# Optimization experiments

Hardware: AMD Instinct MI355X
Metric: run time of the kernel (lower is better)

Reference implementation:

```python
import jax, jax.numpy as jnp
import numpy as np
from jax import lax

DIM = 1152
HEADS = 16
HEAD_DIM = 72  # HEADS*HEAD_DIM == DIM
HID = 4608     # int(DIM*4.0)
B = 2
N = 4096
EPS_RMS = 1e-6
EPS_LA = 1e-15


def setup_inputs() -> dict:
    key = jax.random.key(0)
    ks = jax.random.split(key, 12)
    w = lambda k, shape: (jax.random.normal(k, shape, jnp.float32) * 0.02)
    z = lambda n: jnp.zeros((n,), jnp.float32)
    return {
        "hidden_states": jax.random.normal(ks[0], (B, N, DIM), jnp.float32),
        "temb": jax.random.normal(ks[1], (B, 6 * DIM), jnp.float32),
        "scale_shift_table": jax.random.normal(ks[2], (6, DIM), jnp.float32) / np.float32(np.sqrt(DIM)),
        "Wq": w(ks[3], (DIM, DIM)), "bq": z(DIM),
        "Wk": w(ks[4], (DIM, DIM)), "bk": z(DIM),
        "Wv": w(ks[5], (DIM, DIM)), "bv": z(DIM),
        "Wo": w(ks[6], (DIM, DIM)), "bo": z(DIM),
        "W_inv": w(ks[7], (2 * HID, DIM)), "b_inv": z(2 * HID),   # 1x1 conv dim -> 2*hid
        "W_dw": w(ks[8], (2 * HID, 3)), "b_dw": z(2 * HID),       # depthwise k=3
        "W_pt": w(ks[9], (DIM, HID)),                              # 1x1 conv hid -> dim, no bias
    }


def _rms(x):
    # RMSNorm, elementwise_affine=False, eps=1e-6
    return x * lax.rsqrt(jnp.mean(x * x, axis=-1, keepdims=True) + EPS_RMS)


def reference(hidden_states, temb, scale_shift_table, Wq, bq, Wk, bk, Wv, bv, Wo, bo,
              W_inv, b_inv, W_dw, b_dw, W_pt):
    Bn, Nn, D = hidden_states.shape
    # adaLN-single modulation
    mods = scale_shift_table[None] + temb.reshape(Bn, 6, D)  # (B,6,D)
    shift_msa, scale_msa, gate_msa, shift_mlp, scale_mlp, gate_mlp = (
        mods[:, i][:, None, :] for i in range(6))  # each (B,1,D)

    x = _rms(hidden_states) * (1.0 + scale_msa) + shift_msa

    # --- Lite linear attention (ReLU kernel, denominator via padded-ones value) ---
    q = jax.nn.relu(x @ Wq.T + bq).reshape(Bn, Nn, HEADS, HEAD_DIM).transpose(0, 2, 1, 3)  # bhnd
    k = jax.nn.relu(x @ Wk.T + bk).reshape(Bn, Nn, HEADS, HEAD_DIM).transpose(0, 2, 1, 3)
    v = (x @ Wv.T + bv).reshape(Bn, Nn, HEADS, HEAD_DIM).transpose(0, 2, 1, 3)
    v = jnp.pad(v, ((0, 0), (0, 0), (0, 0), (0, 1)), constant_values=1.0)  # (B,h,N,d+1)
    kv = jnp.einsum('bhnd,bhne->bhde', k, v)        # (B,h,d,d+1)
    out = jnp.einsum('bhnd,bhde->bhne', q, kv)      # (B,h,N,d+1)
    out = out[..., :-1] / (out[..., -1:] + EPS_LA)  # numerator / denominator
    out = out.transpose(0, 2, 1, 3).reshape(Bn, Nn, D)
    attn_out = out @ Wo.T + bo

    hidden_states = gate_msa * attn_out + hidden_states

    # --- GLUMBConv FFN ---
    y = _rms(hidden_states) * (1.0 + scale_mlp) + shift_mlp
    y = jax.nn.silu(y @ W_inv.T + b_inv)            # inverted 1x1 conv + SiLU, (B,N,2*HID)
    yc = y.transpose(0, 2, 1)                        # (B,2*HID,N)
    yc = lax.conv_general_dilated(
        yc, W_dw[:, None, :], window_strides=(1,), padding=[(1, 1)],
        feature_group_count=2 * HID,
        dimension_numbers=('NCH', 'OIH', 'NCH')) + b_dw[None, :, None]
    xg, gate = jnp.split(yc, 2, axis=1)
    y = (xg * jax.nn.silu(gate)).transpose(0, 2, 1)  # (B,N,HID)
    ff = y @ W_pt.T                                   # point conv, no bias

    return hidden_states + gate_mlp * ff
```

## Files before the change

### kernel.cpp

```cpp
#include <hip/hip_runtime.h>
#include <hip/hip_bf16.h>

typedef __hip_bfloat16 bf16;
typedef short short8 __attribute__((ext_vector_type(8)));
typedef float floatx4 __attribute__((ext_vector_type(4)));
typedef int int4v __attribute__((ext_vector_type(4)));

#define DIMC 1152
#define NTOK 8192
#define NSEQ 4096
#define HD 72
#define HDP 73
#define HIDC 4608
#define HID2 9216
#define QKVN 3456
#define KVH (HD * HDP)
#define PZ ((size_t)2048 * DIMC)
#define PZB ((size_t)4096 * DIMC)

#define DP 96
#define KVNT 128
#define KV_NITER 2
#define KV_CHUNKS 16

__device__ __forceinline__ float b2f(bf16 x) { return __bfloat162float(x); }
__device__ __forceinline__ bf16 f2b(float x) { return __float2bfloat16(x); }
__device__ __forceinline__ void st(float* p, float v) { *p = v; }
__device__ __forceinline__ void st(bf16* p, float v)  { *p = f2b(v); }
__device__ __forceinline__ float tf(float x) { return x; }
__device__ __forceinline__ float tf(bf16 x)  { return __bfloat162float(x); }
__device__ __forceinline__ float s2f(short s) {
    unsigned int u = ((unsigned int)(unsigned short)s) << 16;
    return __uint_as_float(u);
}
__device__ __forceinline__ short f2s(float f) {
    bf16 h = f2b(f);
    return *reinterpret_cast<short*>(&h);
}

__device__ __forceinline__ void gload_lds16(const bf16* g, short* l) {
    __builtin_amdgcn_global_load_lds(
        (const __attribute__((address_space(1))) void*)g,
        (__attribute__((address_space(3))) void*)l, 16, 0, 0);
}

__global__ void cvt_all_kernel(const float* __restrict__ s0, const float* __restrict__ s1,
                               const float* __restrict__ s2, const float* __restrict__ s3,
                               const float* __restrict__ s4, const float* __restrict__ s5,
                               bf16* __restrict__ dst) {
    int i = blockIdx.x * 256 + threadIdx.x;
    if (i >= 5308416) return;
    const float* src; int base;
    if (i < 1327104) {
        if (i < 331776)      { src = s0; base = 0; }
        else if (i < 663552) { src = s1; base = 331776; }
        else if (i < 995328) { src = s2; base = 663552; }
        else                 { src = s3; base = 995328; }
    } else if (i < 3981312)  { src = s4; base = 1327104; }
    else                     { src = s5; base = 3981312; }
    floatx4 v = ((const floatx4*)src)[i - base];
    bf16* o = dst + (size_t)i * 4;
    o[0] = f2b(v[0]); o[1] = f2b(v[1]); o[2] = f2b(v[2]); o[3] = f2b(v[3]);
}

__global__ void bias3_kernel(const float* __restrict__ a, const float* __restrict__ b,
                             const float* __restrict__ c, float* __restrict__ o) {
    int i = blockIdx.x * 256 + threadIdx.x;
    if (i < DIMC) { o[i] = a[i]; o[i + DIMC] = b[i]; o[i + 2 * DIMC] = c[i]; }
}

__global__ void mods_kernel(const float* __restrict__ sst, const float* __restrict__ temb,
                            float* __restrict__ mods) {
    int i = blockIdx.x * 256 + threadIdx.x;
    if (i < 2 * 6 * DIMC) {
        int j = i % (6 * DIMC);
        mods[i] = sst[j] + temb[i];
    }
}

template<typename T>
__global__ void rmsmod_kernel(const T* __restrict__ h, const float* __restrict__ mods,
                              int shift_idx, int scale_idx, bf16* __restrict__ xout) {
    int token = blockIdx.x;
    int b = token >> 12;
    int tid = threadIdx.x;
    int wave = tid >> 6, lane = tid & 63;
    const T* hp = h + (size_t)token * DIMC;

    float v[8];
    float s = 0.f;
    if (tid < 144) {
        if constexpr (sizeof(T) == 4) {
            floatx4 a = *(const floatx4*)((const float*)hp + tid * 8);
            floatx4 c = *(const floatx4*)((const float*)hp + tid * 8 + 4);
            v[0]=a[0]; v[1]=a[1]; v[2]=a[2]; v[3]=a[3];
            v[4]=c[0]; v[5]=c[1]; v[6]=c[2]; v[7]=c[3];
        } else {
            short8 a = *(const short8*)((const short*)hp + tid * 8);
            #pragma unroll
            for (int j = 0; j < 8; j++) v[j] = s2f(a[j]);
        }
        #pragma unroll
        for (int j = 0; j < 8; j++) s += v[j] * v[j];
    }
    #pragma unroll
    for (int off = 32; off > 0; off >>= 1) s += __shfl_down(s, off);
    __shared__ float wsum[4];
    if (lane == 0) wsum[wave] = s;
    __syncthreads();
    float tot = wsum[0] + wsum[1] + wsum[2] + wsum[3];
    float r = rsqrtf(tot / (float)DIMC + 1e-6f);

    if (tid < 144) {
        const float* sh = mods + (size_t)(b * 6 + shift_idx) * DIMC + tid * 8;
        const float* sc = mods + (size_t)(b * 6 + scale_idx) * DIMC + tid * 8;
        floatx4 sh0 = *(const floatx4*)sh, sh1 = *(const floatx4*)(sh + 4);
        floatx4 sc0 = *(const floatx4*)sc, sc1 = *(const floatx4*)(sc + 4);
        short8 o;
        o[0] = f2s(v[0] * r * (1.f + sc0[0]) + sh0[0]);
        o[1] = f2s(v[1] * r * (1.f + sc0[1]) + sh0[1]);
        o[2] = f2s(v[2] * r * (1.f + sc0[2]) + sh0[2]);
        o[3] = f2s(v[3] * r * (1.f + sc0[3]) + sh0[3]);
        o[4] = f2s(v[4] * r * (1.f + sc1[0]) + sh1[0]);
        o[5] = f2s(v[5] * r * (1.f + sc1[1]) + sh1[1]);
        o[6] = f2s(v[6] * r * (1.f + sc1[2]) + sh1[2]);
        o[7] = f2s(v[7] * r * (1.f + sc1[3]) + sh1[3]);
        *(short8*)((short*)xout + (size_t)token * DIMC + tid * 8) = o;
    }
}

template<int MODE, typename OT>
__global__ __launch_bounds__(256, 2)
void gemm_kernel(const bf16* __restrict__ A, const bf16* __restrict__ W,
                 const float* __restrict__ bias, const float* __restrict__ mods,
                 int gate_idx, int m_off, const float* __restrict__ resid,
                 OT* __restrict__ out, int N, int Kfull, int Klen,
                 size_t zstride, int bm_lo, int bm_hi) {
    const int bm = blockIdx.x;
    if (bm < bm_lo || bm >= bm_hi) return;
    const int koff = blockIdx.z * Klen;
    __shared__ __align__(16) short As[128 * 64];
    __shared__ __align__(16) short Bs[128 * 64];
    const int tid = threadIdx.x;
    const int wave = tid >> 6;
    const int lane = tid & 63;
    const int quad = lane >> 4;
    const int l16 = lane & 15;
    const int wm = (wave & 1) * 64;
    const int wn = (wave >> 1) * 64;
    const int bn = blockIdx.y;

    floatx4 acc[4][4];
    #pragma unroll
    for (int i = 0; i < 4; i++)
        #pragma unroll
        for (int j = 0; j < 4; j++)
            #pragma unroll
            for (int r = 0; r < 4; r++) acc[i][j][r] = 0.0f;

    const int lrow8 = lane >> 3;
    const int scol = ((lane & 7) ^ lrow8) * 8;
    const bf16* gA = A + (size_t)(bm * 128 + wave * 8 + lrow8) * Kfull + koff + scol;
    const bf16* gB = W + (size_t)(bn * 128 + wave * 8 + lrow8) * Kfull + koff + scol;
    short* lA = &As[wave * 512];
    short* lB = &Bs[wave * 512];
    const size_t rstep = (size_t)32 * Kfull;

    for (int k0 = 0; k0 < Klen; k0 += 64) {
        __syncthreads();
        #pragma unroll
        for (int j = 0; j < 4; j++) gload_lds16(gA + j * rstep + k0, lA + j * 2048);
        #pragma unroll
        for (int j = 0; j < 4; j++) gload_lds16(gB + j * rstep + k0, lB + j * 2048);
        __syncthreads();
        short8 af[2][4], bfr[2][4];
        #pragma unroll
        for (int i = 0; i < 4; i++) {
            const int ra = wm + i * 16 + l16;
            const int rb = wn + i * 16 + l16;
            #pragma unroll
            for (int kk = 0; kk < 2; kk++) {
                af[kk][i]  = *(const short8*)&As[ra * 64 + (((kk * 4 + quad) ^ (ra & 7)) * 8)];
                bfr[kk][i] = *(const short8*)&Bs[rb * 64 + (((kk * 4 + quad) ^ (rb & 7)) * 8)];
            }
        }
        #pragma unroll
        for (int kk = 0; kk < 2; kk++)
            #pragma unroll
            for (int i = 0; i < 4; i++)
                #pragma unroll
                for (int j = 0; j < 4; j++)
                    acc[i][j] = __builtin_amdgcn_mfma_f32_16x16x32_bf16(af[kk][i], bfr[kk][j], acc[i][j], 0, 0, 0);
    }

    #pragma unroll
    for (int i = 0; i < 4; i++) {
        #pragma unroll
        for (int j = 0; j < 4; j++) {
            const int col = bn * 128 + wn + j * 16 + l16;
            #pragma unroll
            for (int r = 0; r < 4; r++) {
                const int m = bm * 128 + wm + i * 16 + quad * 4 + r;
                float v = acc[i][j][r];
                float o;
                if (MODE == 0) {
                    o = v + bias[col];
                    if (col < 2 * DIMC) o = fmaxf(o, 0.f);
                } else if (MODE == 2) {
                    int b = (m + m_off) >> 12;
                    o = mods[(size_t)(b * 6 + gate_idx) * DIMC + col] * (v + bias[col])
                        + resid[(size_t)m * DIMC + col];
                } else if (MODE == 3) {
                    float sv = v + bias[col];
                    o = sv / (1.f + __expf(-sv));
                } else {
                    o = v;
                }
                st(&out[zstride * blockIdx.z + (size_t)m * N + col], o);
            }
        }
    }
}

__global__ void reduce_kernel(const float* __restrict__ part, const bf16* __restrict__ trunk,
                              const float* __restrict__ mods, int b, int r0, size_t pstride,
                              float* __restrict__ out) {
    int i = blockIdx.x * 256 + threadIdx.x;
    int col = i % DIMC;
    float s = part[i] + part[i + pstride] + part[i + 2 * pstride] + part[i + 3 * pstride];
    size_t gidx = ((size_t)b * NSEQ + r0) * DIMC + i;
    float gate = mods[(size_t)(b * 6 + 5) * DIMC + col];
    out[gidx] = b2f(trunk[gidx]) + gate * s;
}

__device__ __forceinline__ int kvaddr(int row, int n) {
    return row * KVNT + ((((n >> 3) ^ (row & 7))) << 3) + (n & 7);
}

__global__ __launch_bounds__(256, 3)
void attn_kv_kernel(const bf16* __restrict__ qkv, float* __restrict__ part) {
    const int chunk = blockIdx.x;
    const int h = blockIdx.y;
    const int b = blockIdx.z;
    __shared__ __align__(16) short kl[DP * KVNT];
    __shared__ __align__(16) short vl[DP * KVNT];
    const int tid = threadIdx.x;
    const int wave = tid >> 6, lane = tid & 63;
    const int quad = lane >> 4, l16 = lane & 15;
    const int wd = (wave & 1) * 48;
    const int we = (wave >> 1) * 48;

    for (int i = tid; i < 24 * KVNT; i += 256) {
        kl[72 * KVNT + i] = 0;
        vl[72 * KVNT + i] = (i < KVNT) ? (short)0x3F80 : (short)0;
    }

    floatx4 acc[3][3];
    #pragma unroll
    for (int i = 0; i < 3; i++)
        #pragma unroll
        for (int j = 0; j < 3; j++)
            #pragma unroll
            for (int r = 0; r < 4; r++) acc[i][j][r] = 0.0f;

    const size_t tok0 = (size_t)b * NSEQ + (size_t)chunk * (KVNT * KV_NITER);
    for (int it = 0; it < KV_NITER; ++it) {
        __syncthreads();
        const short* rb = (const short*)qkv + (tok0 + (size_t)it * KVNT) * QKVN + h * HD;
        #pragma unroll
        for (int p = 0; p < 5; ++p) {
            int idx = p * 256 + tid;
            int o = idx >> 7, n = idx & 127;
            if (o < 9) {
                const short* g = rb + (size_t)n * QKVN + o * 8;
                short8 kk = *(const short8*)(g + DIMC);
                short8 vv = *(const short8*)(g + 2 * DIMC);
                #pragma unroll
                for (int j = 0; j < 8; ++j) {
                    kl[kvaddr(o * 8 + j, n)] = kk[j];
                    vl[kvaddr(o * 8 + j, n)] = vv[j];
                }
            }
        }
        __syncthreads();
        #pragma unroll
        for (int ks = 0; ks < 4; ++ks) {
            const int nb = ks * 32 + quad * 8;
            short8 af[3], bfv[3];
            #pragma unroll
            for (int i = 0; i < 3; ++i) {
                const int ra = wd + i * 16 + l16;
                const int rbn = we + i * 16 + l16;
                af[i]  = *(const short8*)&kl[ra * KVNT + ((((nb >> 3) ^ (ra & 7))) << 3)];
                bfv[i] = *(const short8*)&vl[rbn * KVNT + ((((nb >> 3) ^ (rbn & 7))) << 3)];
            }
            #pragma unroll
            for (int i = 0; i < 3; ++i)
                #pragma unroll
                for (int j = 0; j < 3; ++j)
                    acc[i][j] = __builtin_amdgcn_mfma_f32_16x16x32_bf16(af[i], bfv[j], acc[i][j], 0, 0, 0);
        }
    }

    float* op = part + ((size_t)((b * 16 + h) * KV_CHUNKS + chunk)) * KVH;
    #pragma unroll
    for (int i = 0; i < 3; ++i) {
        const int dbase = wd + i * 16 + quad * 4;
        #pragma unroll
        for (int j = 0; j < 3; ++j) {
            const int e = we + j * 16 + l16;
            if (e < HDP) {
                #pragma unroll
                for (int r = 0; r < 4; ++r) {
                    const int d = dbase + r;
                    if (d < HD) op[d * HDP + e] = acc[i][j][r];
                }
            }
        }
    }
}

__global__ void kvred_kernel(const float* __restrict__ part, float* __restrict__ kvout) {
    int i = blockIdx.x * 256 + threadIdx.x;
    if (i >= 32 * KVH) return;
    int bh = i / KVH, cell = i - bh * KVH;
    const float* p = part + ((size_t)bh * KV_CHUNKS) * KVH + cell;
    float s = 0.f;
    #pragma unroll
    for (int c = 0; c < KV_CHUNKS; ++c) s += p[(size_t)c * KVH];
    kvout[i] = s;
}

__global__ __launch_bounds__(256, 2)
void attn_out_kernel(const bf16* __restrict__ qkv, const float* __restrict__ kv,
                     bf16* __restrict__ outa, int b) {
    int chunk = blockIdx.x;
    int h = blockIdx.y;
    __shared__ float kvt[HDP * HD];
    __shared__ bf16 ql[128 * HD];
    int tid = threadIdx.x;
    for (int i = tid; i < KVH; i += 256) {
        int d = i / HDP, e = i % HDP;
        kvt[e * HD + d] = kv[(size_t)h * KVH + i];
    }
    size_t rowbase = ((size_t)(b * NSEQ) + (size_t)chunk * 128) * QKVN + h * HD;
    for (int idx = tid; idx < 128 * HD; idx += 256) {
        int n = idx / HD, d = idx % HD;
        ql[idx] = qkv[rowbase + (size_t)n * QKVN + d];
    }
    __syncthreads();
    int n = tid >> 1;
    int hf = tid & 1;
    float qr[HD];
    #pragma unroll
    for (int d = 0; d < HD; ++d) qr[d] = b2f(ql[n * HD + d]);
    float den = 0.f;
    #pragma unroll
    for (int d = 0; d < HD; ++d) den += qr[d] * kvt[HD * HD + d];
    den += 1e-15f;
    float inv = 1.0f / den;
    size_t obase = ((size_t)chunk * 128 + n) * DIMC + h * HD;
    for (int ei = 0; ei < 36; ++ei) {
        int e = hf * 36 + ei;
        const float* kr = &kvt[e * HD];
        float s = 0.f;
        #pragma unroll
        for (int d = 0; d < HD; ++d) s += qr[d] * kr[d];
        outa[obase + e] = f2b(s * inv);
    }
}

__global__ __launch_bounds__(576)
void dwglu_kernel(const bf16* __restrict__ ybuf, const float* __restrict__ wdw,
                  const float* __restrict__ bdw, int r0, int rowoff, bf16* __restrict__ outg) {
    int nl = blockIdx.x;
    int g = r0 + nl;
    int c = threadIdx.x * 8;
    int cg = c + HIDC;
    size_t base = (size_t)(nl + rowoff) * HID2;
    const short* yb = (const short*)ybuf;
    short8 zr = {0, 0, 0, 0, 0, 0, 0, 0};
    bool hm = (g > 0), hp = (g < NSEQ - 1);
    short8 xm = hm ? *(const short8*)(yb + base - HID2 + c)  : zr;
    short8 x0 =      *(const short8*)(yb + base + c);
    short8 xp = hp ? *(const short8*)(yb + base + HID2 + c)  : zr;
    short8 gm = hm ? *(const short8*)(yb + base - HID2 + cg) : zr;
    short8 g0 =      *(const short8*)(yb + base + cg);
    short8 gp = hp ? *(const short8*)(yb + base + HID2 + cg) : zr;
    float wx[24], wg[24], bxv[8], bgv[8];
    #pragma unroll
    for (int t = 0; t < 6; t++) {
        *(floatx4*)&wx[t * 4] = *(const floatx4*)(wdw + (size_t)c * 3 + t * 4);
        *(floatx4*)&wg[t * 4] = *(const floatx4*)(wdw + (size_t)cg * 3 + t * 4);
    }
    *(floatx4*)&bxv[0] = *(const floatx4*)(bdw + c);
    *(floatx4*)&bxv[4] = *(const floatx4*)(bdw + c + 4);
    *(floatx4*)&bgv[0] = *(const floatx4*)(bdw + cg);
    *(floatx4*)&bgv[4] = *(const floatx4*)(bdw + cg + 4);
    short8 o;
    #pragma unroll
    for (int j = 0; j < 8; j++) {
        float a  = s2f(xm[j]) * wx[j * 3] + s2f(x0[j]) * wx[j * 3 + 1]
                 + s2f(xp[j]) * wx[j * 3 + 2] + bxv[j];
        float gg = s2f(gm[j]) * wg[j * 3] + s2f(g0[j]) * wg[j * 3 + 1]
                 + s2f(gp[j]) * wg[j * 3 + 2] + bgv[j];
        float sg = gg / (1.f + __expf(-gg));
        o[j] = f2s(a * sg);
    }
    *(short8*)((short*)outg + (size_t)nl * HIDC + c) = o;
}

extern "C" void kernel_launch(void* const* d_in, const int* in_sizes, int n_in,
                              void* d_out, int out_size, void* d_ws, size_t ws_size,
                              hipStream_t stream) {
    const float* h_in = (const float*)d_in[0];
    const float* temb = (const float*)d_in[1];
    const float* sst  = (const float*)d_in[2];
    const float* Wq = (const float*)d_in[3];   const float* bq_ = (const float*)d_in[4];
    const float* Wk = (const float*)d_in[5];   const float* bk_ = (const float*)d_in[6];
    const float* Wv = (const float*)d_in[7];   const float* bv_ = (const float*)d_in[8];
    const float* Wo = (const float*)d_in[9];   const float* bo_ = (const float*)d_in[10];
    const float* Winv = (const float*)d_in[11]; const float* binv = (const float*)d_in[12];
    const float* Wdw  = (const float*)d_in[13]; const float* bdw  = (const float*)d_in[14];
    const float* Wpt  = (const float*)d_in[15];
    float* out = (float*)d_out;

    const int WSMALL = DIMC * DIMC;
    const int WINVN  = HID2 * DIMC;
    const int WPTN   = DIMC * HIDC;

    char* basep = (char*)d_ws;
    size_t off = 0;
    auto alloc = [&](size_t bytes) -> char* {
        char* p = basep + off;
        off += (bytes + 255) & ~(size_t)255;
        return p;
    };
    float* modsb = (float*)alloc((size_t)2 * 6 * DIMC * 4);
    float* kvb   = (float*)alloc((size_t)32 * KVH * 4);
    float* kvpart = (float*)alloc((size_t)32 * KV_CHUNKS * KVH * 4);
    float* bqkv  = (float*)alloc((size_t)QKVN * 4);
    bf16* wqkv = (bf16*)alloc((size_t)3 * WSMALL * 2);
    bf16* wob  = (bf16*)alloc((size_t)WSMALL * 2);
    bf16* wib  = (bf16*)alloc((size_t)WINVN * 2);
    bf16* wpb  = (bf16*)alloc((size_t)WPTN * 2);
    bf16* bx    = (bf16*)alloc((size_t)NTOK * DIMC * 2);
    bf16* trunk = (bf16*)alloc((size_t)NTOK * DIMC * 2);

    const size_t BGLU_B = (size_t)NSEQ * HIDC * 2;
    const size_t BBIG_B = (size_t)NSEQ * HID2 * 2;
    bool bigws = (ws_size >= off + BGLU_B + BBIG_B + 1024);
    char* R = alloc(bigws ? (BGLU_B + BBIG_B) : (size_t)61341696);
    bf16* qkvb = (bf16*)R;

    cvt_all_kernel<<<20736, 256, 0, stream>>>(Wq, Wk, Wv, Wo, Winv, Wpt, wqkv);
    bias3_kernel<<<5, 256, 0, stream>>>(bq_, bk_, bv_, bqkv);
    mods_kernel<<<54, 256, 0, stream>>>(sst, temb, modsb);
    rmsmod_kernel<float><<<NTOK, 256, 0, stream>>>(h_in, modsb, 0, 1, bx);

    gemm_kernel<0, bf16><<<dim3(NTOK / 128, QKVN / 128), 256, 0, stream>>>(
        bx, wqkv, bqkv, nullptr, 0, 0, nullptr, qkvb, QKVN, DIMC, DIMC, 0, 0, 1 << 30);

    attn_kv_kernel<<<dim3(KV_CHUNKS, 16, 2), 256, 0, stream>>>(qkvb, kvpart);
    kvred_kernel<<<(32 * KVH + 255) / 256, 256, 0, stream>>>(kvpart, kvb);
    for (int b = 0; b < 2; ++b) {
        attn_out_kernel<<<dim3(32, 16), 256, 0, stream>>>(qkvb, kvb + (size_t)b * 16 * KVH,
                                                          bx + (size_t)b * NSEQ * DIMC, b);
    }
    gemm_kernel<2, bf16><<<dim3(NTOK / 128, DIMC / 128), 256, 0, stream>>>(
        bx, wob, bo_, modsb, 2, 0, h_in, trunk, DIMC, DIMC, DIMC, 0, 0, 1 << 30);
    rmsmod_kernel<bf16><<<NTOK, 256, 0, stream>>>(trunk, modsb, 3, 4, bx);

    if (bigws) {
        bf16*  bglu = (bf16*)R;
        bf16*  bbig = (bf16*)(R + BGLU_B);
        float* partials = (float*)(R + BGLU_B);
        for (int b = 0; b < 2; ++b) {
            const bf16* Ainv = bx + (size_t)b * NSEQ * DIMC;
            gemm_kernel<3, bf16><<<dim3(NSEQ / 128, HID2 / 128), 256, 0, stream>>>(
                Ainv, wib, binv, nullptr, 0, 0, nullptr, bbig, HID2, DIMC, DIMC, 0, 0, 1 << 30);
            dwglu_kernel<<<dim3(NSEQ), 576, 0, stream>>>(bbig, Wdw, bdw, 0, 0, bglu);
            gemm_kernel<5, float><<<dim3(32, DIMC / 128, 4), 256, 0, stream>>>(
                bglu, wpb, nullptr, nullptr, 0, 0, nullptr, partials, DIMC, HIDC, HIDC / 4,
                PZB, 0, 1 << 30);
            reduce_kernel<<<(int)(PZB / 256), 256, 0, stream>>>(partials, trunk, modsb, b, 0,
                                                                PZB, out);
        }
    } else {
        bf16*  bglu_c   = (bf16*)R;
        bf16*  bbig_c   = (bf16*)(R + (size_t)18874368);
        float* partials = (float*)(R + (size_t)18874368);
        for (int b = 0; b < 2; ++b) {
            for (int c = 0; c < 2; ++c) {
                int r0 = c * 2048;
                int lo = (c == 0) ? 1 : 0;
                int hi = (c == 0) ? 18 : 17;
                const bf16* Ainv = bx + ((size_t)(b * NSEQ + r0)) * DIMC - (size_t)128 * DIMC;
                gemm_kernel<3, bf16><<<dim3(18, HID2 / 128), 256, 0, stream>>>(
                    Ainv, wib, binv, nullptr, 0, 0, nullptr, bbig_c, HID2, DIMC, DIMC, 0, lo, hi);
                dwglu_kernel<<<dim3(2048), 576, 0, stream>>>(bbig_c, Wdw, bdw, r0, 128, bglu_c);
                gemm_kernel<5, float><<<dim3(16, DIMC / 128, 4), 256, 0, stream>>>(
                    bglu_c, wpb, nullptr, nullptr, 0, 0, nullptr, partials, DIMC, HIDC, HIDC / 4,
                    PZ, 0, 1 << 30);
                reduce_kernel<<<(int)(PZ / 256), 256, 0, stream>>>(partials, trunk, modsb, b, r0,
                                                                   PZ, out);
            }
        }
    }
}
```

Baseline: 846.6 us.

## Compute linear-attention output with bf16 MFMA and merge batch launches

Rewrites attn_out_kernel so the q·kv product runs on MFMA 16x16x32 bf16 instructions instead of scalar FP32 loops. Q and the transposed kv matrix are staged in XOR-swizzled shared memory, and the denominator column comes out of the same MFMA tile through a lane shuffle. The two per-batch launches become one launch with a z-dimension. The cost is that kv is rounded to bf16, which lowers accuracy, but this kernel is a small part of the total runtime.

```diff
diff --git a/kernel.cpp b/kernel.cpp
--- a/kernel.cpp
+++ b/kernel.cpp
@@ -333,40 +333,84 @@
 
 __global__ __launch_bounds__(256, 2)
 void attn_out_kernel(const bf16* __restrict__ qkv, const float* __restrict__ kv,
-                     bf16* __restrict__ outa, int b) {
-    int chunk = blockIdx.x;
-    int h = blockIdx.y;
-    __shared__ float kvt[HDP * HD];
-    __shared__ bf16 ql[128 * HD];
-    int tid = threadIdx.x;
-    for (int i = tid; i < KVH; i += 256) {
-        int d = i / HDP, e = i % HDP;
-        kvt[e * HD + d] = kv[(size_t)h * KVH + i];
-    }
-    size_t rowbase = ((size_t)(b * NSEQ) + (size_t)chunk * 128) * QKVN + h * HD;
-    for (int idx = tid; idx < 128 * HD; idx += 256) {
-        int n = idx / HD, d = idx % HD;
-        ql[idx] = qkv[rowbase + (size_t)n * QKVN + d];
+                     bf16* __restrict__ outa) {
+    const int chunk = blockIdx.x;
+    const int h = blockIdx.y;
+    const int b = blockIdx.z;
+    __shared__ __align__(16) short ql[128 * 128];
+    __shared__ __align__(16) short kvt[80 * 128];
+    const int tid = threadIdx.x;
+    const int wave = tid >> 6, lane = tid & 63;
+    const int quad = lane >> 4, l16 = lane & 15;
+    const int wm = wave * 32;
+
+    const short* qbase = (const short*)qkv + ((size_t)(b * NSEQ) + (size_t)chunk * 128) * QKVN + h * HD;
+    #pragma unroll
+    for (int t = 0; t < 8; ++t) {
+        int idx = t * 256 + tid;
+        int o = idx >> 7, n = idx & 127;
+        short8 vv = {0, 0, 0, 0, 0, 0, 0, 0};
+        if (o < 9) vv = *(const short8*)(qbase + (size_t)n * QKVN + o * 8);
+        *(short8*)&ql[n * 128 + ((o ^ (n & 7)) << 3)] = vv;
+    }
+    const float* kp = kv + (size_t)(b * 16 + h) * KVH;
+    #pragma unroll
+    for (int t = 0; t < 5; ++t) {
+        int idx = t * 256 + tid;
+        int o = idx / 80, e = idx - (idx / 80) * 80;
+        short8 vv = {0, 0, 0, 0, 0, 0, 0, 0};
+        if (e < HDP && o < 9) {
+            #pragma unroll
+            for (int j = 0; j < 8; ++j) {
+                int d = o * 8 + j;
+                if (d < HD) vv[j] = f2s(kp[(size_t)d * HDP + e]);
+            }
+        }
+        *(short8*)&kvt[e * 128 + ((o ^ (e & 7)) << 3)] = vv;
     }
     __syncthreads();
-    int n = tid >> 1;
-    int hf = tid & 1;
-    float qr[HD];
-    #pragma unroll
-    for (int d = 0; d < HD; ++d) qr[d] = b2f(ql[n * HD + d]);
-    float den = 0.f;
-    #pragma unroll
-    for (int d = 0; d < HD; ++d) den += qr[d] * kvt[HD * HD + d];
-    den += 1e-15f;
-    float inv = 1.0f / den;
-    size_t obase = ((size_t)chunk * 128 + n) * DIMC + h * HD;
-    for (int ei = 0; ei < 36; ++ei) {
-        int e = hf * 36 + ei;
-        const float* kr = &kvt[e * HD];
-        float s = 0.f;
-        #pragma unroll
-        for (int d = 0; d < HD; ++d) s += qr[d] * kr[d];
-        outa[obase + e] = f2b(s * inv);
+
+    floatx4 acc[2][5];
+    #pragma unroll
+    for (int i = 0; i < 2; ++i)
+        #pragma unroll
+        for (int j = 0; j < 5; ++j)
+            #pragma unroll
+            for (int r = 0; r < 4; ++r) acc[i][j][r] = 0.0f;
+
+    #pragma unroll
+    for (int kk = 0; kk < 3; ++kk) {
+        const int s = kk * 4 + quad;
+        short8 af[2];
+        #pragma unroll
+        for (int i = 0; i < 2; ++i) {
+            const int ra = wm + i * 16 + l16;
+            af[i] = *(const short8*)&ql[ra * 128 + ((s ^ (ra & 7)) << 3)];
+        }
+        #pragma unroll
+        for (int j = 0; j < 5; ++j) {
+            const int rb = j * 16 + l16;
+            short8 bfv = *(const short8*)&kvt[rb * 128 + ((s ^ (rb & 7)) << 3)];
+            #pragma unroll
+            for (int i = 0; i < 2; ++i)
+                acc[i][j] = __builtin_amdgcn_mfma_f32_16x16x32_bf16(af[i], bfv, acc[i][j], 0, 0, 0);
+        }
+    }
+
+    #pragma unroll
+    for (int i = 0; i < 2; ++i) {
+        #pragma unroll
+        for (int r = 0; r < 4; ++r) {
+            float den = __shfl(acc[i][4][r], (lane & 48) | 8);
+            float inv = 1.0f / (den + 1e-15f);
+            const int m = wm + i * 16 + quad * 4 + r;
+            bf16* op = outa + ((size_t)(b * NSEQ) + (size_t)chunk * 128 + m) * DIMC + h * HD;
+            #pragma unroll
+            for (int j = 0; j < 5; ++j) {
+                const int e = j * 16 + l16;
+                if (e < HD) op[e] = f2b(acc[i][j][r] * inv);
+            }
+        }
     }
 }
 
@@ -463,10 +507,7 @@
 
     attn_kv_kernel<<<dim3(KV_CHUNKS, 16, 2), 256, 0, stream>>>(qkvb, kvpart);
     kvred_kernel<<<(32 * KVH + 255) / 256, 256, 0, stream>>>(kvpart, kvb);
-    for (int b = 0; b < 2; ++b) {
-        attn_out_kernel<<<dim3(32, 16), 256, 0, stream>>>(qkvb, kvb + (size_t)b * 16 * KVH,
-                                                          bx + (size_t)b * NSEQ * DIMC, b);
-    }
+    attn_out_kernel<<<dim3(32, 16, 2), 256, 0, stream>>>(qkvb, kvb, bx);
     gemm_kernel<2, bf16><<<dim3(NTOK / 128, DIMC / 128), 256, 0, stream>>>(
         bx, wob, bo_, modsb, 2, 0, h_in, trunk, DIMC, DIMC, DIMC, 0, 0, 1 << 30);
     rmsmod_kernel<bf16><<<NTOK, 256, 0, stream>>>(trunk, modsb, 3, 4, bx);
```

Result: faster. 812.9 us (-4.0%).
